# Optimization experiments

Measured on AMD Instinct MI355X. Metric: run time of the kernel, lower is better.

Reference implementation:

```python
import jax, jax.numpy as jnp
import numpy as np
from jax import lax

RATIOS = (0.5, 1.0, 2.0)
SCALES = (8, 16, 32)
BASE = 16
STRIDE = 16
N_PRE = 6000
N_POST = 300      # post-NMS proposals kept
NMS_THRESH = 0.7
MIN_SIZE = 16.0


def _anchor_base():
    x = y = BASE / 2.0
    ab = np.zeros((len(RATIOS) * len(SCALES), 4), np.float32)
    for i, r in enumerate(RATIOS):
        for j, s in enumerate(SCALES):
            h = BASE * s * np.sqrt(r)
            w = BASE * s * np.sqrt(1.0 / r)
            k = i * len(SCALES) + j
            ab[k] = [y - h / 2, x - w / 2, y + h / 2, x + w / 2]
    return ab


def _anchors(h, w):
    ab = _anchor_base()
    sy = np.arange(0, h * STRIDE, STRIDE)
    sx = np.arange(0, w * STRIDE, STRIDE)
    sx, sy = np.meshgrid(sx, sy)
    shift = np.stack((sy.ravel(), sx.ravel(), sy.ravel(), sx.ravel()), axis=1)
    # [K, A, 4] -> [K*A, 4], row-major over (y, x) pixels matching NHWC flatten
    return (ab[None, :, :] + shift[:, None, :]).reshape(-1, 4).astype(np.float32)


def _conv(x, w, b, pad):
    y = lax.conv_general_dilated(x, w, (1, 1), ((pad, pad), (pad, pad)),
                                 dimension_numbers=('NCHW', 'OIHW', 'NCHW'))
    return y + b[None, :, None, None]


def _loc2bbox(anchor, loc):
    h = anchor[:, 2] - anchor[:, 0]
    w = anchor[:, 3] - anchor[:, 1]
    cy = anchor[:, 0] + 0.5 * h
    cx = anchor[:, 1] + 0.5 * w
    dy, dx, dh, dw = loc[:, 0], loc[:, 1], loc[:, 2], loc[:, 3]
    ncy = dy * h + cy
    ncx = dx * w + cx
    nh = jnp.exp(dh) * h
    nw = jnp.exp(dw) * w
    return jnp.stack([ncy - 0.5 * nh, ncx - 0.5 * nw, ncy + 0.5 * nh, ncx + 0.5 * nw], axis=1)


def _iou(b):
    tl = jnp.maximum(b[:, None, :2], b[None, :, :2])
    br = jnp.minimum(b[:, None, 2:], b[None, :, 2:])
    wh = jnp.clip(br - tl, 0.0)
    inter = wh[..., 0] * wh[..., 1]
    area = (b[:, 2] - b[:, 0]) * (b[:, 3] - b[:, 1])
    return inter / (area[:, None] + area[None, :] - inter + 1e-9)


def _nms_keep(iou):
    # greedy NMS over score-sorted boxes: suppress later boxes overlapping kept earlier ones
    n = iou.shape[0]
    idx = jnp.arange(n)
    def step(keep, i):
        sup = (iou[i] > NMS_THRESH) & (idx > i) & keep[i]
        return keep & (~sup), None
    keep, _ = lax.scan(step, jnp.ones((n,), dtype=bool), idx)
    return keep


def _proposal(loc, fg, anchor, img_h, img_w, scale=1.0):
    boxes = _loc2bbox(anchor, loc)
    boxes = jnp.stack([jnp.clip(boxes[:, 0], 0.0, img_h),
                       jnp.clip(boxes[:, 1], 0.0, img_w),
                       jnp.clip(boxes[:, 2], 0.0, img_h),
                       jnp.clip(boxes[:, 3], 0.0, img_w)], axis=1)
    hs = boxes[:, 2] - boxes[:, 0]
    ws = boxes[:, 3] - boxes[:, 1]
    ms = MIN_SIZE * scale
    score = jnp.where((hs >= ms) & (ws >= ms), fg, -jnp.inf)
    top, idx = lax.top_k(score, N_PRE)
    bk = boxes[idx]                                    # [N_PRE, 4]
    keep = _nms_keep(_iou(lax.stop_gradient(bk)))      # selection is non-differentiable
    fs = jnp.where(keep, top, -jnp.inf)
    _, o2 = lax.top_k(fs, N_POST)
    return bk[o2]                                      # [N_POST, 4]


def setup_inputs() -> dict:
    key = jax.random.key(0)
    ks = jax.random.split(key, 4)
    C, H, W = 512, 50, 76
    return {
        "feature": jax.random.normal(ks[0], (1, C, H, W), jnp.float32),
        "conv1_w": jax.random.normal(ks[1], (512, C, 3, 3), jnp.float32) * 0.01,
        "conv1_b": jnp.zeros((512,), jnp.float32),
        "score_w": jax.random.normal(ks[2], (18, 512, 1, 1), jnp.float32) * 0.01,
        "score_b": jnp.zeros((18,), jnp.float32),
        "loc_w": jax.random.normal(ks[3], (36, 512, 1, 1), jnp.float32) * 0.01,
        "loc_b": jnp.zeros((36,), jnp.float32),
        "img_h": 800,
        "img_w": 1216,
    }


def reference(feature, conv1_w, conv1_b, score_w, score_b, loc_w, loc_b, img_h, img_w):
    _, c, h, w = feature.shape
    A = 9
    anchor = jnp.asarray(_anchors(h, w))
    x = jax.nn.relu(_conv(feature, conv1_w, conv1_b, 1))
    locs = _conv(x, loc_w, loc_b, 0)
    rpn_locs = locs.transpose(0, 2, 3, 1).reshape(1, -1, 4)
    sc = _conv(x, score_w, score_b, 0).transpose(0, 2, 3, 1)   # [1, h, w, 2A]
    sm = jax.nn.softmax(sc.reshape(1, h, w, A, 2), axis=-1)
    fg = sm[..., 1].reshape(-1)
    rpn_scores = sc.reshape(1, -1, 2)
    rois = _proposal(rpn_locs[0], fg, anchor, float(img_h), float(img_w), scale=1.0)
    return rpn_locs, rpn_scores, rois, anchor
```

## Files before the change

kernel.cpp:

```cpp
#include <hip/hip_runtime.h>

#define HH 50
#define WW2 76
#define NPIX 3800
#define CIN 512
#define NANCH 34200
#define NPRE 6000
#define NPOST 300
#define WPR 94

typedef unsigned long long u64;
typedef unsigned int u32;

__device__ __forceinline__ int PADL(int i) { return i + (i >> 4); }

template <bool DOW>
__global__ __launch_bounds__(256) void rpn_wtrans(const float* __restrict__ wgt,
                                                  float* __restrict__ wt,
                                                  const float* __restrict__ sw,
                                                  const float* __restrict__ lw,
                                                  float* __restrict__ wt2,
                                                  u32* __restrict__ hist,
                                                  u32* __restrict__ info) {
    __shared__ float tile[32][33];
    const int bx = blockIdx.x;
    const int by = blockIdx.y;
    const int t  = threadIdx.x;
    const int tx = t & 31, ty = t >> 5;
    int gid = (by * 144 + bx) * 256 + t;
    if (gid < 65536) hist[gid] = 0u;
    else if (gid < 65552) info[gid - 65536] = 0u;
    if (gid < 32768) {
        int c = gid >> 6, n = gid & 63;
        float v = 0.f;
        if (n < 18) v = sw[n * 512 + c];
        else if (n < 54) v = lw[(n - 18) * 512 + c];
        wt2[((c >> 2) * 64 + n) * 4 + (c & 3)] = v;
    }
    if (!DOW) return;
#pragma unroll
    for (int r = 0; r < 32; r += 8) {
        int ko = by * 32 + ty + r;
        tile[ty + r][tx] = wgt[(size_t)ko * 4608 + bx * 32 + tx];
    }
    __syncthreads();
#pragma unroll
    for (int r = 0; r < 32; r += 8) {
        int cit = bx * 32 + ty + r;
        wt[(size_t)cit * 512 + by * 32 + tx] = tile[tx][ty + r];
    }
}

template <bool USEWT>
__global__ __launch_bounds__(256, 2) void rpn_conv1(
    const float* __restrict__ feat, const float* __restrict__ wsrc,
    float* __restrict__ Xpt, int cin_blk, int czbase) {
    const int yb = blockIdx.x;
    const int kg = blockIdx.y;
    const int cz = blockIdx.z + czbase;
    const int t  = threadIdx.x;
    const int kp = t & 15;
    const int ty = t >> 4;
    const int row  = ty >> 2;
    const int xseg = ty & 3;
    const int x0 = xseg * 19;
    __shared__ float in_l[2048];
    __shared__ float w_l[2304];

    const int y0 = yb * 4 - 1;
    int inSrc[8]; u32 inValid = 0, inPad = 0;
#pragma unroll
    for (int k = 0; k < 8; ++k) {
        int q = t + k * 256;
        int c = q / 504, rem = q - c * 504;
        int r = rem / 84, xx = rem - r * 84;
        int gy = y0 + r, gx = xx - 1;
        bool inb = q < 2016;
        bool ok = inb && ((unsigned)gy < 50u) && ((unsigned)gx < 76u);
        inSrc[k] = c * NPIX + gy * 76 + gx;
        if (ok) inValid |= (1u << k);
        else if (inb) inPad |= (1u << k);
    }
#pragma unroll
    for (int k = 0; k < 8; ++k)
        if ((inPad >> k) & 1) in_l[t + k * 256] = 0.f;

    const float* wb;
    int wOffA = 0;
    int wSrc[9];
    if (USEWT) {
        wb = wsrc + (size_t)(cz * cin_blk) * 9 * 512 + kg * 64;
        wOffA = 8 * t - 7 * (t & 63);
    } else {
        wb = wsrc + (size_t)(kg * 64) * 4608 + (size_t)(cz * cin_blk) * 9;
#pragma unroll
        for (int k = 0; k < 9; ++k) {
            int q = t + k * 256;
            int c = q / 576, r2 = q - c * 576;
            int tap = r2 >> 6, ko = r2 & 63;
            wSrc[k] = ko * 4608 + c * 9 + tap;
        }
    }

    const float* fb = feat + (size_t)(cz * cin_blk) * NPIX;
    float acc[4][19];
#pragma unroll
    for (int o = 0; o < 4; ++o)
#pragma unroll
        for (int p = 0; p < 19; ++p) acc[o][p] = 0.f;

    const int niter = cin_blk >> 2;
#pragma unroll 1
    for (int it = 0; it < niter; ++it) {
        __syncthreads();
#pragma unroll
        for (int k = 0; k < 8; ++k)
            if ((inValid >> k) & 1) in_l[t + k * 256] = fb[inSrc[k]];
        if (USEWT) {
#pragma unroll
            for (int k = 0; k < 9; ++k)
                w_l[t + k * 256] = wb[wOffA + k * 2048];
        } else {
#pragma unroll
            for (int k = 0; k < 9; ++k)
                w_l[t + k * 256] = wb[wSrc[k]];
        }
        __syncthreads();
#pragma unroll 1
        for (int c = 0; c < 4; ++c) {
            const float* ir0 = &in_l[(c * 6 + row) * 84 + x0];
            const float* wl  = &w_l[c * 576 + 4 * kp];
#pragma unroll
            for (int r = 0; r < 3; ++r) {
                const float* ir = ir0 + r * 84;
                float win[21];
#pragma unroll
                for (int w = 0; w < 21; ++w) win[w] = ir[w];
                float wv[4][3];
#pragma unroll
                for (int tp = 0; tp < 3; ++tp) {
                    const float* wr = wl + (r * 3 + tp) * 64;
#pragma unroll
                    for (int o = 0; o < 4; ++o) wv[o][tp] = wr[o];
                }
#pragma unroll
                for (int p = 0; p < 19; ++p) {
#pragma unroll
                    for (int o = 0; o < 4; ++o) {
                        acc[o][p] = fmaf(wv[o][0], win[p],     acc[o][p]);
                        acc[o][p] = fmaf(wv[o][1], win[p + 1], acc[o][p]);
                        acc[o][p] = fmaf(wv[o][2], win[p + 2], acc[o][p]);
                    }
                }
            }
        }
        fb += 4 * NPIX;
        wb += USEWT ? 4 * 9 * 512 : 36;
    }

    const int k0 = kg * 64 + 4 * kp;
    const int y = yb * 4 + row;
    if (y < 50) {
        float* d0 = Xpt + ((size_t)cz * NPIX + y * 76 + x0) * 512 + k0;
#pragma unroll
        for (int p = 0; p < 19; ++p)
            *reinterpret_cast<float4*>(d0 + (size_t)p * 512) =
                make_float4(acc[0][p], acc[1][p], acc[2][p], acc[3][p]);
    }
}

__global__ __launch_bounds__(64) void rpn_head(
    const float* __restrict__ Xpt, const float* __restrict__ wt2,
    const float* __restrict__ b1,
    const float* __restrict__ sb, const float* __restrict__ lb,
    const int* __restrict__ ihp, const int* __restrict__ iwp,
    float* __restrict__ out, float* __restrict__ boxes,
    u32* __restrict__ keys, u32* __restrict__ hist, int nz) {
    const int p0 = blockIdx.x * 8;
    const int t  = threadIdx.x;
    __shared__ __align__(16) float xs[8 * 512];
    __shared__ float ovl[8][64];
    float4* dst = reinterpret_cast<float4*>(xs);
#pragma unroll
    for (int i = 0; i < 16; ++i) {
        int idx = t + i * 64;
        int px = idx >> 7, cc = idx & 127;
        float4 v = *reinterpret_cast<const float4*>(b1 + cc * 4);
        const float* src = Xpt + ((size_t)(p0 + px)) * 512 + cc * 4;
        for (int z = 0; z < nz; ++z) {
            float4 x = *reinterpret_cast<const float4*>(src + (size_t)z * NPIX * 512);
            v.x += x.x; v.y += x.y; v.z += x.z; v.w += x.w;
        }
        v.x = fmaxf(v.x, 0.f); v.y = fmaxf(v.y, 0.f);
        v.z = fmaxf(v.z, 0.f); v.w = fmaxf(v.w, 0.f);
        dst[idx] = v;
    }
    __syncthreads();
    float acc[8];
    {
        float b = (t < 18) ? sb[t] : ((t < 54) ? lb[t - 18] : 0.f);
#pragma unroll
        for (int px = 0; px < 8; ++px) acc[px] = b;
    }
    const float4* wv = reinterpret_cast<const float4*>(wt2) + t;
#pragma unroll 4
    for (int c4 = 0; c4 < 128; ++c4) {
        float4 w = wv[c4 * 64];
#pragma unroll
        for (int px = 0; px < 8; ++px) {
            float4 x = *reinterpret_cast<const float4*>(xs + px * 512 + c4 * 4);
            acc[px] = fmaf(w.x, x.x, acc[px]);
            acc[px] = fmaf(w.y, x.y, acc[px]);
            acc[px] = fmaf(w.z, x.z, acc[px]);
            acc[px] = fmaf(w.w, x.w, acc[px]);
        }
    }
#pragma unroll
    for (int px = 0; px < 8; ++px) ovl[px][t] = acc[px];
    __syncthreads();
    const float ch = (float)(*ihp), cw = (float)(*iwp);
#pragma unroll
    for (int pass = 0; pass < 2; ++pass) {
        int a, px;
        bool act;
        if (pass == 0) { act = (t < 63); px = t / 9; a = t - px * 9; }
        else           { act = (t < 9);  px = 7;     a = t; }
        if (act) {
            const int p = p0 + px;
            const float* ov = ovl[px];
            const float s0 = ov[2 * a], s1 = ov[2 * a + 1];
            const float dy = ov[18 + 4 * a], dx = ov[18 + 4 * a + 1];
            const float dh = ov[18 + 4 * a + 2], dw = ov[18 + 4 * a + 3];
            const int yy = p / WW2, xx = p % WW2;
            const int ai = p * 9 + a;
            *reinterpret_cast<float4*>(out + ai * 4) = make_float4(dy, dx, dh, dw);
            *reinterpret_cast<float2*>(out + 136800 + ai * 2) = make_float2(s0, s1);
            double r  = (a < 3) ? 0.5 : (a < 6) ? 1.0 : 2.0;
            int m3 = a % 3;
            double s2 = (m3 == 0) ? 8.0 : (m3 == 1) ? 16.0 : 32.0;
            double hd = (16.0 * s2) * sqrt(r);
            double wd = (16.0 * s2) * sqrt(1.0 / r);
            float ay1 = (float)(8.0 - hd * 0.5), ax1 = (float)(8.0 - wd * 0.5);
            float ay2 = (float)(8.0 + hd * 0.5), ax2 = (float)(8.0 + wd * 0.5);
            float fy = (float)(yy * 16), fx = (float)(xx * 16);
            float A0 = ay1 + fy, A1 = ax1 + fx, A2 = ay2 + fy, A3 = ax2 + fx;
            *reinterpret_cast<float4*>(out + 206400 + ai * 4) = make_float4(A0, A1, A2, A3);
            float ah = __fsub_rn(A2, A0), aw = __fsub_rn(A3, A1);
            float cy = __fadd_rn(A0, __fmul_rn(0.5f, ah));
            float cx = __fadd_rn(A1, __fmul_rn(0.5f, aw));
            float ncy = __fadd_rn(__fmul_rn(dy, ah), cy);
            float ncx = __fadd_rn(__fmul_rn(dx, aw), cx);
            float nh = __fmul_rn(expf(dh), ah);
            float nw = __fmul_rn(expf(dw), aw);
            float b0 = __fsub_rn(ncy, __fmul_rn(0.5f, nh));
            float b1v = __fsub_rn(ncx, __fmul_rn(0.5f, nw));
            float b2 = __fadd_rn(ncy, __fmul_rn(0.5f, nh));
            float b3 = __fadd_rn(ncx, __fmul_rn(0.5f, nw));
            b0 = fminf(fmaxf(b0, 0.f), ch); b2 = fminf(fmaxf(b2, 0.f), ch);
            b1v = fminf(fmaxf(b1v, 0.f), cw); b3 = fminf(fmaxf(b3, 0.f), cw);
            float hs = __fsub_rn(b2, b0), wsz = __fsub_rn(b3, b1v);
            float m = fmaxf(s0, s1);
            float e0 = expf(__fsub_rn(s0, m)), e1 = expf(__fsub_rn(s1, m));
            float fg = __fdiv_rn(e1, __fadd_rn(e0, e1));
            float score = (hs >= 16.f && wsz >= 16.f) ? fg : -__builtin_inff();
            *reinterpret_cast<float4*>(boxes + ai * 4) = make_float4(b0, b1v, b2, b3);
            u32 kb = __float_as_uint(score);
            kb = (kb & 0x80000000u) ? ~kb : (kb | 0x80000000u);
            keys[ai] = kb;
            atomicAdd(&hist[kb >> 16], 1u);
        }
    }
}

__global__ __launch_bounds__(1024) void rpn_threshsel(const u32* __restrict__ hist,
                                                      u32* __restrict__ info,
                                                      const u32* __restrict__ keys,
                                                      u64* __restrict__ selk) {
    __shared__ u32 tmp[1024];
    __shared__ u32 part[256], h2[256];
    __shared__ int segs;
    __shared__ u32 Tsh;
    const int t = threadIdx.x;
    {
        u32 s = 0;
        const u32* hp = hist + t * 64;
#pragma unroll 8
        for (int b = 0; b < 64; ++b) s += hp[b];
        tmp[t] = s;
    }
    __syncthreads();
    if (t < 256) part[t] = tmp[4 * t] + tmp[4 * t + 1] + tmp[4 * t + 2] + tmp[4 * t + 3];
    __syncthreads();
    for (int off = 1; off < 256; off <<= 1) {
        u32 v = 0, add = 0;
        if (t < 256) { v = part[t]; add = (t + off < 256) ? part[t + off] : 0u; }
        __syncthreads();
        if (t < 256) part[t] = v + add;
        __syncthreads();
    }
    if (t < 256) {
        u32 suf  = part[t];
        u32 sufn = (t < 255) ? part[t + 1] : 0u;
        if (suf >= NPRE && sufn < NPRE) segs = t;
    }
    __syncthreads();
    const int seg = segs;
    const u32 above = (seg < 255) ? part[seg + 1] : 0u;
    if (t < 256) h2[t] = hist[seg * 256 + t];
    __syncthreads();
    for (int off = 1; off < 256; off <<= 1) {
        u32 v = 0, add = 0;
        if (t < 256) { v = h2[t]; add = (t + off < 256) ? h2[t + off] : 0u; }
        __syncthreads();
        if (t < 256) h2[t] = v + add;
        __syncthreads();
    }
    if (t < 256) {
        u32 tot  = above + h2[t];
        u32 totn = above + ((t < 255) ? h2[t + 1] : 0u);
        if (tot >= NPRE && totn < NPRE) Tsh = (u32)(seg * 256 + t);
    }
    __syncthreads();
    const u32 T = Tsh;
    const int lane = t & 63;
    for (int base = 0; base < NANCH; base += 1024) {
        int idx = base + t;
        u32 k = (idx < NANCH) ? keys[idx] : 0u;
        bool sel = (idx < NANCH) && ((k >> 16) >= T);
        u64 ball = __ballot(sel);
        u32 wbase = 0;
        if (lane == 0 && ball) wbase = atomicAdd(&info[2], (u32)__popcll(ball));
        wbase = __shfl(wbase, 0);
        if (sel) {
            u32 pos = wbase + (u32)__popcll(ball & ((1ull << lane) - 1ull));
            if (pos < 8192) selk[pos] = ((u64)k << 32) | (u64)(0xFFFFFFFFu - (u32)idx);
        }
    }
}

__global__ __launch_bounds__(1024) void rpn_sort_local(u64* __restrict__ selk,
                                                       const u32* __restrict__ info) {
    __shared__ u64 s[2176];
    const int t = threadIdx.x;
    const int seg = blockIdx.x;
    const int base = seg * 2048;
    int n = (int)info[2]; if (n > 8192) n = 8192;
    for (int i = t; i < 2048; i += 1024)
        s[PADL(i)] = (base + i < n) ? selk[base + i] : 0ull;
    __syncthreads();
    const bool D = ((seg & 1) == 0);
    for (int k = 2; k <= 2048; k <<= 1) {
        for (int j = k >> 1; j > 0; j >>= 1) {
            int p1 = ((t & ~(j - 1)) << 1) | (t & (j - 1));
            int p2 = p1 | j;
            bool desc = (((p1 & k) == 0) == D);
            u64 A = s[PADL(p1)], B = s[PADL(p2)];
            if (desc ? (A < B) : (A > B)) { s[PADL(p1)] = B; s[PADL(p2)] = A; }
            __syncthreads();
        }
    }
    for (int i = t; i < 2048; i += 1024) selk[base + i] = s[PADL(i)];
}

__global__ __launch_bounds__(512) void rpn_sort_gpass(u64* __restrict__ selk,
                                                      int k, int j) {
    int i = blockIdx.x * 512 + threadIdx.x;
    int p1 = ((i & ~(j - 1)) << 1) | (i & (j - 1));
    int p2 = p1 | j;
    bool desc = ((p1 & k) == 0);
    u64 A = selk[p1], B = selk[p2];
    if (desc ? (A < B) : (A > B)) { selk[p1] = B; selk[p2] = A; }
}

template <bool FINAL>
__global__ __launch_bounds__(1024) void rpn_sort_lmerge(u64* __restrict__ selk, int k,
                                                        const float* __restrict__ boxes,
                                                        float* __restrict__ bk) {
    __shared__ u64 s[2176];
    const int t = threadIdx.x;
    const int base = blockIdx.x * 2048;
    for (int i = t; i < 2048; i += 1024) s[PADL(i)] = selk[base + i];
    __syncthreads();
    const bool desc = ((base & k) == 0);
    for (int j = 1024; j > 0; j >>= 1) {
        int p1 = ((t & ~(j - 1)) << 1) | (t & (j - 1));
        int p2 = p1 | j;
        u64 A = s[PADL(p1)], B = s[PADL(p2)];
        if (desc ? (A < B) : (A > B)) { s[PADL(p1)] = B; s[PADL(p2)] = A; }
        __syncthreads();
    }
    if (FINAL) {
        for (int i = t; i < 2048; i += 1024) {
            int r = base + i;
            if (r < NPRE) {
                u32 oi = 0xFFFFFFFFu - (u32)(s[PADL(i)] & 0xFFFFFFFFull);
                if (oi >= NANCH) oi = 0;
                reinterpret_cast<float4*>(bk)[r] = reinterpret_cast<const float4*>(boxes)[oi];
            }
        }
    } else {
        for (int i = t; i < 2048; i += 1024) selk[base + i] = s[PADL(i)];
    }
}

__global__ __launch_bounds__(64) void rpn_iou(const float* __restrict__ bk,
                                              u64* __restrict__ mask) {
    const int t = threadIdx.x;
    const int bj = blockIdx.x, bi = blockIdx.y;
    const int j0 = bj * 64;
    const int i = bi * 64 + t;
    if (j0 + 63 <= bi * 64) {
        if (i < NPRE) mask[(size_t)i * WPR + bj] = 0ull;
        return;
    }
    __shared__ float4 jb[64];
    jb[t] = (j0 + t < NPRE) ? reinterpret_cast<const float4*>(bk)[j0 + t]
                            : make_float4(0.f, 0.f, 0.f, 0.f);
    __syncthreads();
    if (i >= NPRE) return;
    float4 b = reinterpret_cast<const float4*>(bk)[i];
    float areai = __fmul_rn(__fsub_rn(b.z, b.x), __fsub_rn(b.w, b.y));
    u64 bits = 0ull;
    for (int jj = 0; jj < 64; ++jj) {
        int j = j0 + jj;
        if (j <= i || j >= NPRE) continue;
        float4 c = jb[jj];
        float ty = fmaxf(b.x, c.x), tx = fmaxf(b.y, c.y);
        float by = fminf(b.z, c.z), bx2 = fminf(b.w, c.w);
        float ih = fmaxf(__fsub_rn(by, ty), 0.f);
        float iw = fmaxf(__fsub_rn(bx2, tx), 0.f);
        float inter = __fmul_rn(ih, iw);
        float areaj = __fmul_rn(__fsub_rn(c.z, c.x), __fsub_rn(c.w, c.y));
        float denom = __fadd_rn(__fsub_rn(__fadd_rn(areai, areaj), inter), 1e-9f);
        float iou = __fdiv_rn(inter, denom);
        if (iou > 0.7f) bits |= (1ull << jj);
    }
    mask[(size_t)i * WPR + bj] = bits;
}

__global__ __launch_bounds__(64) void rpn_nms(const u64* __restrict__ mask,
                                              const float* __restrict__ bk,
                                              float* __restrict__ rois) {
    const int lane = threadIdx.x;
    u64 rem0 = 0ull, rem1 = 0ull, curW = 0ull;
    __shared__ unsigned short klist[304];
    int kcnt = 0;
    u64 pm0[16], pm1[16], pmg[16];
#pragma unroll
    for (int u = 0; u < 16; ++u) {
        pm0[u] = mask[(size_t)u * WPR + lane];
        pm1[u] = (lane < 30) ? mask[(size_t)u * WPR + 64 + lane] : 0ull;
        pmg[u] = mask[(size_t)u * WPR + 0];
    }
    bool done = false;
    for (int base = 0; base < NPRE && !done; base += 16) {
        if ((base & 63) == 0) {
            int w = base >> 6;
            curW = (w < 64) ? __shfl(rem0, w) : __shfl(rem1, w - 64);
        }
#pragma unroll
        for (int u = 0; u < 16; ++u) {
            const int i = base + u;
            u64 m0 = pm0[u], m1 = pm1[u], mg = pmg[u];
            const int ni = i + 16;
            pm0[u] = mask[(size_t)ni * WPR + lane];
            pm1[u] = (lane < 30) ? mask[(size_t)ni * WPR + 64 + lane] : 0ull;
            pmg[u] = mask[(size_t)ni * WPR + (ni >> 6)];
            if (((curW >> (i & 63)) & 1ull) == 0ull) {
                rem0 |= m0;
                rem1 |= m1;
                curW |= mg;
                if (lane == 0 && kcnt < 304) klist[kcnt] = (unsigned short)i;
                ++kcnt;
                if (kcnt >= NPOST) { done = true; break; }
            }
        }
    }
    __syncthreads();
    const int nk = kcnt < NPOST ? kcnt : NPOST;
    for (int r = lane; r < nk; r += 64) {
        int bi = klist[r];
        reinterpret_cast<float4*>(rois)[r] = reinterpret_cast<const float4*>(bk)[bi];
    }
    if (kcnt < NPOST) {
        int pos = kcnt;
        for (int i = 0; i < NPRE && pos < NPOST; ++i) {
            int w = i >> 6;
            u64 wv = (w < 64) ? __shfl(rem0, w) : __shfl(rem1, w - 64);
            if ((wv >> (i & 63)) & 1ull) {
                if (lane < 4) rois[pos * 4 + lane] = bk[i * 4 + lane];
                ++pos;
            }
        }
    }
}

extern "C" void kernel_launch(void* const* d_in, const int* in_sizes, int n_in,
                              void* d_out, int out_size, void* d_ws, size_t ws_size,
                              hipStream_t stream) {
    (void)in_sizes; (void)n_in; (void)out_size;
    const float* feat = (const float*)d_in[0];
    const float* w1   = (const float*)d_in[1];
    const float* b1   = (const float*)d_in[2];
    const float* sw   = (const float*)d_in[3];
    const float* sb   = (const float*)d_in[4];
    const float* lw   = (const float*)d_in[5];
    const float* lb   = (const float*)d_in[6];
    const int*   ih   = (const int*)d_in[7];
    const int*   iw   = (const int*)d_in[8];
    float* out = (float*)d_out;

    const size_t WT_B    = 9437184;
    const size_t WT2_B   = 131072;
    const size_t REST_B  = WT2_B + 547200 + 136800 + 262144 + 64 + 65536 + 96000 + 4528128;
    const size_t SLICE_B = (size_t)512 * NPIX * 4;
    int nz; bool usewt;
    if      (ws_size >= 8 * SLICE_B + WT_B + REST_B) { nz = 8; usewt = true; }
    else if (ws_size >= 4 * SLICE_B + WT_B + REST_B) { nz = 4; usewt = true; }
    else if (ws_size >= 2 * SLICE_B + WT_B + REST_B) { nz = 2; usewt = true; }
    else                                             { nz = 2; usewt = false; }

    char* p = (char*)d_ws;
    float* Xpt = (float*)p;          p += (size_t)nz * SLICE_B;
    float* wt = nullptr;
    if (usewt) { wt = (float*)p;     p += WT_B; }
    float* wt2    = (float*)p;       p += WT2_B;
    float* boxes  = (float*)p;       p += 547200;
    u32*   keys   = (u32*)p;         p += 136800;
    u32*   hist   = (u32*)p;         p += 262144;
    u32*   info   = (u32*)p;         p += 64;
    u64*   selk   = (u64*)p;         p += 65536;
    float* bk     = (float*)p;       p += 96000;
    u64*   mask   = (u64*)p;

    const int cin_blk = 512 / nz;
    const int half = nz / 2;

    if (usewt) {
        rpn_wtrans<true><<<dim3(144, 16), 256, 0, stream>>>(w1, wt, sw, lw, wt2, hist, info);
        rpn_conv1<true><<<dim3(13, 8, half), 256, 0, stream>>>(feat, wt, Xpt, cin_blk, 0);
        rpn_conv1<true><<<dim3(13, 8, nz - half), 256, 0, stream>>>(feat, wt, Xpt, cin_blk, half);
    } else {
        rpn_wtrans<false><<<dim3(144, 16), 256, 0, stream>>>(w1, nullptr, sw, lw, wt2, hist, info);
        rpn_conv1<false><<<dim3(13, 8, half), 256, 0, stream>>>(feat, w1, Xpt, cin_blk, 0);
        rpn_conv1<false><<<dim3(13, 8, nz - half), 256, 0, stream>>>(feat, w1, Xpt, cin_blk, half);
    }
    rpn_head<<<475, 64, 0, stream>>>(Xpt, wt2, b1, sb, lb, ih, iw, out, boxes, keys, hist, nz);
    rpn_threshsel<<<1, 1024, 0, stream>>>(hist, info, keys, selk);
    rpn_sort_local<<<4, 1024, 0, stream>>>(selk, info);
    rpn_sort_gpass<<<8, 512, 0, stream>>>(selk, 4096, 2048);
    rpn_sort_lmerge<false><<<4, 1024, 0, stream>>>(selk, 4096, nullptr, nullptr);
    rpn_sort_gpass<<<8, 512, 0, stream>>>(selk, 8192, 4096);
    rpn_sort_gpass<<<8, 512, 0, stream>>>(selk, 8192, 2048);
    rpn_sort_lmerge<true><<<4, 1024, 0, stream>>>(selk, 8192, boxes, bk);
    rpn_iou<<<dim3(WPR, WPR), 64, 0, stream>>>(bk, mask);
    rpn_nms<<<1, 64, 0, stream>>>(mask, bk, out + 205200);
}
```

Measured before the change: 613.0 us.

## Widen head and IoU kernels to 256 threads and merge conv1 launches

The RPN head kernel now uses four wavefronts per block, with each wave computing two pixels instead of one wave computing all eight, and the post-processing runs in a single 72-thread pass. The IoU mask kernel packs four row-tiles per 256-thread block so the shared column tile is loaded once for all four. The two split conv1 launches are merged into one launch over all input-channel slices. The aim is to raise per-block parallelism and cut launch overhead, at the cost of more threads idling in the head's output phase and an early return placed after a barrier in the IoU kernel.

```diff
diff --git a/kernel.cpp b/kernel.cpp
--- a/kernel.cpp
+++ b/kernel.cpp
@@ -169,7 +169,7 @@
     }
 }
 
-__global__ __launch_bounds__(64) void rpn_head(
+__global__ __launch_bounds__(256) void rpn_head(
     const float* __restrict__ Xpt, const float* __restrict__ wt2,
     const float* __restrict__ b1,
     const float* __restrict__ sb, const float* __restrict__ lb,
@@ -182,8 +182,8 @@
     __shared__ float ovl[8][64];
     float4* dst = reinterpret_cast<float4*>(xs);
 #pragma unroll
-    for (int i = 0; i < 16; ++i) {
-        int idx = t + i * 64;
+    for (int i = 0; i < 4; ++i) {
+        int idx = t + i * 256;
         int px = idx >> 7, cc = idx & 127;
         float4 v = *reinterpret_cast<const float4*>(b1 + cc * 4);
         const float* src = Xpt + ((size_t)(p0 + px)) * 512 + cc * 4;
@@ -196,79 +196,72 @@
         dst[idx] = v;
     }
     __syncthreads();
-    float acc[8];
+    const int w = t >> 6, lane = t & 63;
+    float a0, a1;
     {
-        float b = (t < 18) ? sb[t] : ((t < 54) ? lb[t - 18] : 0.f);
-#pragma unroll
-        for (int px = 0; px < 8; ++px) acc[px] = b;
-    }
-    const float4* wv = reinterpret_cast<const float4*>(wt2) + t;
+        float b = (lane < 18) ? sb[lane] : ((lane < 54) ? lb[lane - 18] : 0.f);
+        a0 = b; a1 = b;
+    }
+    const float4* wv = reinterpret_cast<const float4*>(wt2) + lane;
+    const float* x0b = xs + (2 * w) * 512;
+    const float* x1b = xs + (2 * w + 1) * 512;
 #pragma unroll 4
     for (int c4 = 0; c4 < 128; ++c4) {
-        float4 w = wv[c4 * 64];
-#pragma unroll
-        for (int px = 0; px < 8; ++px) {
-            float4 x = *reinterpret_cast<const float4*>(xs + px * 512 + c4 * 4);
-            acc[px] = fmaf(w.x, x.x, acc[px]);
-            acc[px] = fmaf(w.y, x.y, acc[px]);
-            acc[px] = fmaf(w.z, x.z, acc[px]);
-            acc[px] = fmaf(w.w, x.w, acc[px]);
-        }
-    }
-#pragma unroll
-    for (int px = 0; px < 8; ++px) ovl[px][t] = acc[px];
-    __syncthreads();
-    const float ch = (float)(*ihp), cw = (float)(*iwp);
-#pragma unroll
-    for (int pass = 0; pass < 2; ++pass) {
-        int a, px;
-        bool act;
-        if (pass == 0) { act = (t < 63); px = t / 9; a = t - px * 9; }
-        else           { act = (t < 9);  px = 7;     a = t; }
-        if (act) {
-            const int p = p0 + px;
-            const float* ov = ovl[px];
-            const float s0 = ov[2 * a], s1 = ov[2 * a + 1];
-            const float dy = ov[18 + 4 * a], dx = ov[18 + 4 * a + 1];
-            const float dh = ov[18 + 4 * a + 2], dw = ov[18 + 4 * a + 3];
-            const int yy = p / WW2, xx = p % WW2;
-            const int ai = p * 9 + a;
-            *reinterpret_cast<float4*>(out + ai * 4) = make_float4(dy, dx, dh, dw);
-            *reinterpret_cast<float2*>(out + 136800 + ai * 2) = make_float2(s0, s1);
-            double r  = (a < 3) ? 0.5 : (a < 6) ? 1.0 : 2.0;
-            int m3 = a % 3;
-            double s2 = (m3 == 0) ? 8.0 : (m3 == 1) ? 16.0 : 32.0;
-            double hd = (16.0 * s2) * sqrt(r);
-            double wd = (16.0 * s2) * sqrt(1.0 / r);
-            float ay1 = (float)(8.0 - hd * 0.5), ax1 = (float)(8.0 - wd * 0.5);
-            float ay2 = (float)(8.0 + hd * 0.5), ax2 = (float)(8.0 + wd * 0.5);
-            float fy = (float)(yy * 16), fx = (float)(xx * 16);
-            float A0 = ay1 + fy, A1 = ax1 + fx, A2 = ay2 + fy, A3 = ax2 + fx;
-            *reinterpret_cast<float4*>(out + 206400 + ai * 4) = make_float4(A0, A1, A2, A3);
-            float ah = __fsub_rn(A2, A0), aw = __fsub_rn(A3, A1);
-            float cy = __fadd_rn(A0, __fmul_rn(0.5f, ah));
-            float cx = __fadd_rn(A1, __fmul_rn(0.5f, aw));
-            float ncy = __fadd_rn(__fmul_rn(dy, ah), cy);
-            float ncx = __fadd_rn(__fmul_rn(dx, aw), cx);
-            float nh = __fmul_rn(expf(dh), ah);
-            float nw = __fmul_rn(expf(dw), aw);
-            float b0 = __fsub_rn(ncy, __fmul_rn(0.5f, nh));
-            float b1v = __fsub_rn(ncx, __fmul_rn(0.5f, nw));
-            float b2 = __fadd_rn(ncy, __fmul_rn(0.5f, nh));
-            float b3 = __fadd_rn(ncx, __fmul_rn(0.5f, nw));
-            b0 = fminf(fmaxf(b0, 0.f), ch); b2 = fminf(fmaxf(b2, 0.f), ch);
-            b1v = fminf(fmaxf(b1v, 0.f), cw); b3 = fminf(fmaxf(b3, 0.f), cw);
-            float hs = __fsub_rn(b2, b0), wsz = __fsub_rn(b3, b1v);
-            float m = fmaxf(s0, s1);
-            float e0 = expf(__fsub_rn(s0, m)), e1 = expf(__fsub_rn(s1, m));
-            float fg = __fdiv_rn(e1, __fadd_rn(e0, e1));
-            float score = (hs >= 16.f && wsz >= 16.f) ? fg : -__builtin_inff();
-            *reinterpret_cast<float4*>(boxes + ai * 4) = make_float4(b0, b1v, b2, b3);
-            u32 kb = __float_as_uint(score);
-            kb = (kb & 0x80000000u) ? ~kb : (kb | 0x80000000u);
-            keys[ai] = kb;
-            atomicAdd(&hist[kb >> 16], 1u);
-        }
+        float4 wq = wv[c4 * 64];
+        float4 xa = *reinterpret_cast<const float4*>(x0b + c4 * 4);
+        float4 xb = *reinterpret_cast<const float4*>(x1b + c4 * 4);
+        a0 = fmaf(wq.x, xa.x, a0); a0 = fmaf(wq.y, xa.y, a0);
+        a0 = fmaf(wq.z, xa.z, a0); a0 = fmaf(wq.w, xa.w, a0);
+        a1 = fmaf(wq.x, xb.x, a1); a1 = fmaf(wq.y, xb.y, a1);
+        a1 = fmaf(wq.z, xb.z, a1); a1 = fmaf(wq.w, xb.w, a1);
+    }
+    if (lane < 54) { ovl[2 * w][lane] = a0; ovl[2 * w + 1][lane] = a1; }
+    __syncthreads();
+    if (t < 72) {
+        const int px = t / 9, a = t - px * 9;
+        const float ch = (float)(*ihp), cw = (float)(*iwp);
+        const int p = p0 + px;
+        const float* ov = ovl[px];
+        const float s0 = ov[2 * a], s1 = ov[2 * a + 1];
+        const float dy = ov[18 + 4 * a], dx = ov[18 + 4 * a + 1];
+        const float dh = ov[18 + 4 * a + 2], dw = ov[18 + 4 * a + 3];
+        const int yy = p / WW2, xx = p % WW2;
+        const int ai = p * 9 + a;
+        *reinterpret_cast<float4*>(out + ai * 4) = make_float4(dy, dx, dh, dw);
+        *reinterpret_cast<float2*>(out + 136800 + ai * 2) = make_float2(s0, s1);
+        double r  = (a < 3) ? 0.5 : (a < 6) ? 1.0 : 2.0;
+        int m3 = a % 3;
+        double s2 = (m3 == 0) ? 8.0 : (m3 == 1) ? 16.0 : 32.0;
+        double hd = (16.0 * s2) * sqrt(r);
+        double wd = (16.0 * s2) * sqrt(1.0 / r);
+        float ay1 = (float)(8.0 - hd * 0.5), ax1 = (float)(8.0 - wd * 0.5);
+        float ay2 = (float)(8.0 + hd * 0.5), ax2 = (float)(8.0 + wd * 0.5);
+        float fy = (float)(yy * 16), fx = (float)(xx * 16);
+        float A0 = ay1 + fy, A1 = ax1 + fx, A2 = ay2 + fy, A3 = ax2 + fx;
+        *reinterpret_cast<float4*>(out + 206400 + ai * 4) = make_float4(A0, A1, A2, A3);
+        float ah = __fsub_rn(A2, A0), aw = __fsub_rn(A3, A1);
+        float cy = __fadd_rn(A0, __fmul_rn(0.5f, ah));
+        float cx = __fadd_rn(A1, __fmul_rn(0.5f, aw));
+        float ncy = __fadd_rn(__fmul_rn(dy, ah), cy);
+        float ncx = __fadd_rn(__fmul_rn(dx, aw), cx);
+        float nh = __fmul_rn(expf(dh), ah);
+        float nw = __fmul_rn(expf(dw), aw);
+        float b0 = __fsub_rn(ncy, __fmul_rn(0.5f, nh));
+        float b1v = __fsub_rn(ncx, __fmul_rn(0.5f, nw));
+        float b2 = __fadd_rn(ncy, __fmul_rn(0.5f, nh));
+        float b3 = __fadd_rn(ncx, __fmul_rn(0.5f, nw));
+        b0 = fminf(fmaxf(b0, 0.f), ch); b2 = fminf(fmaxf(b2, 0.f), ch);
+        b1v = fminf(fmaxf(b1v, 0.f), cw); b3 = fminf(fmaxf(b3, 0.f), cw);
+        float hs = __fsub_rn(b2, b0), wsz = __fsub_rn(b3, b1v);
+        float m = fmaxf(s0, s1);
+        float e0 = expf(__fsub_rn(s0, m)), e1 = expf(__fsub_rn(s1, m));
+        float fg = __fdiv_rn(e1, __fadd_rn(e0, e1));
+        float score = (hs >= 16.f && wsz >= 16.f) ? fg : -__builtin_inff();
+        *reinterpret_cast<float4*>(boxes + ai * 4) = make_float4(b0, b1v, b2, b3);
+        u32 kb = __float_as_uint(score);
+        kb = (kb & 0x80000000u) ? ~kb : (kb | 0x80000000u);
+        keys[ai] = kb;
+        atomicAdd(&hist[kb >> 16], 1u);
     }
 }
 
@@ -403,20 +396,23 @@
     }
 }
 
-__global__ __launch_bounds__(64) void rpn_iou(const float* __restrict__ bk,
-                                              u64* __restrict__ mask) {
+__global__ __launch_bounds__(256) void rpn_iou(const float* __restrict__ bk,
+                                               u64* __restrict__ mask) {
     const int t = threadIdx.x;
-    const int bj = blockIdx.x, bi = blockIdx.y;
+    const int lane = t & 63, w = t >> 6;
+    const int bj = blockIdx.x;
+    const int bi = blockIdx.y * 4 + w;
     const int j0 = bj * 64;
-    const int i = bi * 64 + t;
+    __shared__ float4 jb[64];
+    if (t < 64) jb[t] = (j0 + t < NPRE) ? reinterpret_cast<const float4*>(bk)[j0 + t]
+                                        : make_float4(0.f, 0.f, 0.f, 0.f);
+    __syncthreads();
+    if (bi >= WPR) return;
+    const int i = bi * 64 + lane;
     if (j0 + 63 <= bi * 64) {
         if (i < NPRE) mask[(size_t)i * WPR + bj] = 0ull;
         return;
     }
-    __shared__ float4 jb[64];
-    jb[t] = (j0 + t < NPRE) ? reinterpret_cast<const float4*>(bk)[j0 + t]
-                            : make_float4(0.f, 0.f, 0.f, 0.f);
-    __syncthreads();
     if (i >= NPRE) return;
     float4 b = reinterpret_cast<const float4*>(bk)[i];
     float areai = __fmul_rn(__fsub_rn(b.z, b.x), __fsub_rn(b.w, b.y));
@@ -534,18 +530,15 @@
     u64*   mask   = (u64*)p;
 
     const int cin_blk = 512 / nz;
-    const int half = nz / 2;
 
     if (usewt) {
         rpn_wtrans<true><<<dim3(144, 16), 256, 0, stream>>>(w1, wt, sw, lw, wt2, hist, info);
-        rpn_conv1<true><<<dim3(13, 8, half), 256, 0, stream>>>(feat, wt, Xpt, cin_blk, 0);
-        rpn_conv1<true><<<dim3(13, 8, nz - half), 256, 0, stream>>>(feat, wt, Xpt, cin_blk, half);
+        rpn_conv1<true><<<dim3(13, 8, nz), 256, 0, stream>>>(feat, wt, Xpt, cin_blk, 0);
     } else {
         rpn_wtrans<false><<<dim3(144, 16), 256, 0, stream>>>(w1, nullptr, sw, lw, wt2, hist, info);
-        rpn_conv1<false><<<dim3(13, 8, half), 256, 0, stream>>>(feat, w1, Xpt, cin_blk, 0);
-        rpn_conv1<false><<<dim3(13, 8, nz - half), 256, 0, stream>>>(feat, w1, Xpt, cin_blk, half);
-    }
-    rpn_head<<<475, 64, 0, stream>>>(Xpt, wt2, b1, sb, lb, ih, iw, out, boxes, keys, hist, nz);
+        rpn_conv1<false><<<dim3(13, 8, nz), 256, 0, stream>>>(feat, w1, Xpt, cin_blk, 0);
+    }
+    rpn_head<<<475, 256, 0, stream>>>(Xpt, wt2, b1, sb, lb, ih, iw, out, boxes, keys, hist, nz);
     rpn_threshsel<<<1, 1024, 0, stream>>>(hist, info, keys, selk);
     rpn_sort_local<<<4, 1024, 0, stream>>>(selk, info);
     rpn_sort_gpass<<<8, 512, 0, stream>>>(selk, 4096, 2048);
@@ -553,6 +546,6 @@
     rpn_sort_gpass<<<8, 512, 0, stream>>>(selk, 8192, 4096);
     rpn_sort_gpass<<<8, 512, 0, stream>>>(selk, 8192, 2048);
     rpn_sort_lmerge<true><<<4, 1024, 0, stream>>>(selk, 8192, boxes, bk);
-    rpn_iou<<<dim3(WPR, WPR), 64, 0, stream>>>(bk, mask);
+    rpn_iou<<<dim3(WPR, 24), 256, 0, stream>>>(bk, mask);
     rpn_nms<<<1, 64, 0, stream>>>(mask, bk, out + 205200);
 }
```

Result: faster. 575.5 us (median of 3 runs) (-6.1%).
